# Kernel optimization log

Measured on AMD Instinct MI355X. Metric: run time of the kernel, lower is better.

The kernel has to match this reference:

```python
import jax, jax.numpy as jnp
import numpy as np

TOKENS = 4096
IN_FEATURES = 4096
OUT_FEATURES = 4096
NNZ = 512  # nonzeros per output row, multiple of 4 so vectorize-pad is a no-op


def setup_inputs() -> dict:
    key = jax.random.key(0)
    k1, k2, k3, k4 = jax.random.split(key, 4)
    x = jax.random.normal(k1, (TOKENS, IN_FEATURES), dtype=jnp.float32)
    w = jax.random.normal(k2, (OUT_FEATURES, NNZ), dtype=jnp.float32)
    # sorted per-row column indices, mimicking nonzero() order of a pruned row
    mask = jnp.sort(
        jax.random.randint(k3, (OUT_FEATURES, NNZ), 0, IN_FEATURES, dtype=jnp.int32),
        axis=-1,
    )
    b = jax.random.normal(k4, (OUT_FEATURES,), dtype=jnp.float32)
    return {"input": x, "condensed_weight": w, "input_mask": mask, "bias": b}


def reference(input, condensed_weight, input_mask, bias):
    # y[t, o] = sum_k input[t, input_mask[o, k]] * condensed_weight[o, k] + bias[o]
    # Scatter condensed rows back to a dense [O, In] weight, then GEMM.
    # .add handles duplicate / padded (index 0, weight 0) entries exactly like
    # the gather-multiply-reduce formulation.
    O, K = condensed_weight.shape
    In = input.shape[-1]
    rows = jnp.arange(O, dtype=input_mask.dtype)[:, None]  # [O, 1]
    W = jnp.zeros((O, In), dtype=condensed_weight.dtype).at[rows, input_mask].add(condensed_weight)
    return input @ W.T + bias
```

## Files before the change

### kernel.cpp

```cpp
#include <hip/hip_runtime.h>
#include <hip/hip_bf16.h>
#include <stdint.h>

#define TOKENS 4096
#define IN_F   4096
#define OUT_F  4096
#define NNZ    512

using floatx4 = __attribute__((ext_vector_type(4))) float;
using bf16x8  = __attribute__((ext_vector_type(8))) __bf16;

__device__ __forceinline__ unsigned short f2bf(float f) {
    unsigned int u = __float_as_uint(f);
    u += 0x7FFFu + ((u >> 16) & 1u);
    return (unsigned short)(u >> 16);
}

__global__ __launch_bounds__(256) void prep_fused(
        const float* __restrict__ x,
        const float* __restrict__ w,
        const int*   __restrict__ mask,
        unsigned short* __restrict__ Xb,
        unsigned short* __restrict__ Wb) {
    __shared__ unsigned short row[IN_F];
    const int b = blockIdx.x;
    const int t = threadIdx.x;

    if (b < OUT_F) {
        uint4* rv = (uint4*)row;
        rv[t]       = make_uint4(0u, 0u, 0u, 0u);
        rv[t + 256] = make_uint4(0u, 0u, 0u, 0u);
        __syncthreads();

        const int base = b * NNZ;
#pragma unroll
        for (int e = 0; e < 2; ++e) {
            const int k = t + e * 256;
            const int idx = mask[base + k];
            if (k == 0 || mask[base + k - 1] != idx) {
                float s = w[base + k];
                int j = k + 1;
                while (j < NNZ && mask[base + j] == idx) { s += w[base + j]; ++j; }
                row[idx] = f2bf(s);
            }
        }
        __syncthreads();

        uint4* out = (uint4*)(Wb + (size_t)b * IN_F);
        out[t]       = rv[t];
        out[t + 256] = rv[t + 256];
    } else {
        const int i = (b - OUT_F) * 256 + t;
        const float4* xv = (const float4*)x;
        float4 a = xv[2 * i];
        float4 c = xv[2 * i + 1];
        uint4 o;
        o.x = (unsigned)f2bf(a.x) | ((unsigned)f2bf(a.y) << 16);
        o.y = (unsigned)f2bf(a.z) | ((unsigned)f2bf(a.w) << 16);
        o.z = (unsigned)f2bf(c.x) | ((unsigned)f2bf(c.y) << 16);
        o.w = (unsigned)f2bf(c.z) | ((unsigned)f2bf(c.w) << 16);
        ((uint4*)Xb)[i] = o;
    }
}

__global__ __launch_bounds__(256) void gemm_bt_bias(
        const unsigned short* __restrict__ A,
        const unsigned short* __restrict__ B,
        const float* __restrict__ bias,
        float* __restrict__ C) {
    __shared__ unsigned short As[128 * 64];
    __shared__ unsigned short Bs[128 * 64];

    const int tid  = threadIdx.x;
    const int wave = tid >> 6;
    const int lane = tid & 63;
    const int m0 = blockIdx.y * 128;
    const int n0 = blockIdx.x * 128;
    const int wm = (wave >> 1) * 64;
    const int wn = (wave & 1) * 64;

    floatx4 acc[4][4] = {};

    const int lrow = lane >> 3;
    const int kseg = (lane & 7) ^ lrow;
    const int lq   = lane >> 4;
    const int lm   = lane & 15;
    const int lm7  = lm & 7;

    for (int k0 = 0; k0 < IN_F; k0 += 64) {
#pragma unroll
        for (int i = 0; i < 4; ++i) {
            const int cb  = (i * 4 + wave);
            const int row = cb * 8 + lrow;
            const unsigned short* ga =
                A + (size_t)(m0 + row) * IN_F + k0 + kseg * 8;
            const unsigned short* gb =
                B + (size_t)(n0 + row) * IN_F + k0 + kseg * 8;
            __builtin_amdgcn_global_load_lds(
                (__attribute__((address_space(1))) void*)ga,
                (__attribute__((address_space(3))) void*)(As + cb * 512),
                16, 0, 0);
            __builtin_amdgcn_global_load_lds(
                (__attribute__((address_space(1))) void*)gb,
                (__attribute__((address_space(3))) void*)(Bs + cb * 512),
                16, 0, 0);
        }
        __syncthreads();

#pragma unroll
        for (int ks = 0; ks < 2; ++ks) {
            bf16x8 af[4], bfr[4];
#pragma unroll
            for (int mi = 0; mi < 4; ++mi) {
                const int chunk = (ks * 4 + lq) ^ lm7;
                af[mi] = *(const bf16x8*)(As + (wm + mi * 16 + lm) * 64 + chunk * 8);
            }
#pragma unroll
            for (int ni = 0; ni < 4; ++ni) {
                const int chunk = (ks * 4 + lq) ^ lm7;
                bfr[ni] = *(const bf16x8*)(Bs + (wn + ni * 16 + lm) * 64 + chunk * 8);
            }
#pragma unroll
            for (int mi = 0; mi < 4; ++mi)
#pragma unroll
                for (int ni = 0; ni < 4; ++ni)
                    acc[mi][ni] = __builtin_amdgcn_mfma_f32_16x16x32_bf16(
                        af[mi], bfr[ni], acc[mi][ni], 0, 0, 0);
        }
        __syncthreads();
    }

#pragma unroll
    for (int ni = 0; ni < 4; ++ni) {
        const int n = n0 + wn + ni * 16 + lm;
        const float bv = bias[n];
#pragma unroll
        for (int mi = 0; mi < 4; ++mi) {
            const int mbase = m0 + wm + mi * 16 + lq * 4;
#pragma unroll
            for (int r = 0; r < 4; ++r) {
                C[(size_t)(mbase + r) * OUT_F + n] = acc[mi][ni][r] + bv;
            }
        }
    }
}

extern "C" void kernel_launch(void* const* d_in, const int* in_sizes, int n_in,
                              void* d_out, int out_size, void* d_ws, size_t ws_size,
                              hipStream_t stream) {
    const float* x    = (const float*)d_in[0];
    const float* w    = (const float*)d_in[1];
    const int*   mask = (const int*)d_in[2];
    const float* bias = (const float*)d_in[3];
    float* out = (float*)d_out;

    unsigned short* Xb = (unsigned short*)d_ws;
    unsigned short* Wb = Xb + (size_t)TOKENS * IN_F;

    prep_fused<<<OUT_F + 8192, 256, 0, stream>>>(x, w, mask, Xb, Wb);
    dim3 grid(32, 32);
    gemm_bt_bias<<<grid, 256, 0, stream>>>(Xb, Wb, bias, out);
}
```

Baseline: 281.2 us.

## Rewrite GEMM as 256x256 tile, 8-wave, double-buffered pipelined MFMA kernel

Measured after the change: 253.8 us. 1.11x faster.

```diff
diff --git a/kernel.cpp b/kernel.cpp
--- a/kernel.cpp
+++ b/kernel.cpp
@@ -63,83 +63,178 @@
     }
 }
 
-__global__ __launch_bounds__(256) void gemm_bt_bias(
+
+#define GLL16(src, dst) \
+    __builtin_amdgcn_global_load_lds((__attribute__((address_space(1))) void*)(src), \
+                                     (__attribute__((address_space(3))) void*)(dst), 16, 0, 0)
+
+__global__ __launch_bounds__(512, 2) void gemm_bt_bias(
         const unsigned short* __restrict__ A,
         const unsigned short* __restrict__ B,
         const float* __restrict__ bias,
         float* __restrict__ C) {
-    __shared__ unsigned short As[128 * 64];
-    __shared__ unsigned short Bs[128 * 64];
+    __shared__ unsigned short As[2][16384];
+    __shared__ unsigned short Bs[2][16384];
 
     const int tid  = threadIdx.x;
     const int wave = tid >> 6;
     const int lane = tid & 63;
-    const int m0 = blockIdx.y * 128;
-    const int n0 = blockIdx.x * 128;
-    const int wm = (wave >> 1) * 64;
-    const int wn = (wave & 1) * 64;
-
-    floatx4 acc[4][4] = {};
-
-    const int lrow = lane >> 3;
-    const int kseg = (lane & 7) ^ lrow;
     const int lq   = lane >> 4;
     const int lm   = lane & 15;
     const int lm7  = lm & 7;
-
-    for (int k0 = 0; k0 < IN_F; k0 += 64) {
-#pragma unroll
-        for (int i = 0; i < 4; ++i) {
-            const int cb  = (i * 4 + wave);
-            const int row = cb * 8 + lrow;
-            const unsigned short* ga =
-                A + (size_t)(m0 + row) * IN_F + k0 + kseg * 8;
-            const unsigned short* gb =
-                B + (size_t)(n0 + row) * IN_F + k0 + kseg * 8;
-            __builtin_amdgcn_global_load_lds(
-                (__attribute__((address_space(1))) void*)ga,
-                (__attribute__((address_space(3))) void*)(As + cb * 512),
-                16, 0, 0);
-            __builtin_amdgcn_global_load_lds(
-                (__attribute__((address_space(1))) void*)gb,
-                (__attribute__((address_space(3))) void*)(Bs + cb * 512),
-                16, 0, 0);
-        }
-        __syncthreads();
-
-#pragma unroll
-        for (int ks = 0; ks < 2; ++ks) {
-            bf16x8 af[4], bfr[4];
-#pragma unroll
-            for (int mi = 0; mi < 4; ++mi) {
-                const int chunk = (ks * 4 + lq) ^ lm7;
-                af[mi] = *(const bf16x8*)(As + (wm + mi * 16 + lm) * 64 + chunk * 8);
-            }
-#pragma unroll
-            for (int ni = 0; ni < 4; ++ni) {
-                const int chunk = (ks * 4 + lq) ^ lm7;
-                bfr[ni] = *(const bf16x8*)(Bs + (wn + ni * 16 + lm) * 64 + chunk * 8);
-            }
-#pragma unroll
-            for (int mi = 0; mi < 4; ++mi)
-#pragma unroll
-                for (int ni = 0; ni < 4; ++ni)
-                    acc[mi][ni] = __builtin_amdgcn_mfma_f32_16x16x32_bf16(
-                        af[mi], bfr[ni], acc[mi][ni], 0, 0, 0);
-        }
-        __syncthreads();
+    const int wm2  = wave >> 2;
+    const int wn4  = wave & 3;
+
+    const int bid = blockIdx.x;
+    const int swz = (bid & 7) * 32 + (bid >> 3);
+    const int m0  = (swz >> 4) << 8;
+    const int n0  = (swz & 15) << 8;
+
+    const int r   = tid >> 3;
+    const int cse = ((tid & 7) ^ (r & 7)) * 8;
+    const int oAX0 = (m0 + r)       * IN_F + cse;
+    const int oAX1 = (m0 + 128 + r) * IN_F + cse;
+    const int oAY0 = (m0 +  64 + r) * IN_F + cse;
+    const int oAY1 = (m0 + 192 + r) * IN_F + cse;
+    const int bc_  = (r >> 5) * 64 + (r & 31);
+    const int oBU0 = (n0 + bc_)        * IN_F + cse;
+    const int oBU1 = (n0 + 128 + bc_)  * IN_F + cse;
+    const int oBV0 = (n0 +  32 + bc_)  * IN_F + cse;
+    const int oBV1 = (n0 + 160 + bc_)  * IN_F + cse;
+    const int wofs = wave * 512;
+
+#define STAGE_AX(bb, kk) { GLL16(A + oAX0 + (kk), &As[bb][        wofs]); \
+                           GLL16(A + oAX1 + (kk), &As[bb][ 4096 + wofs]); }
+#define STAGE_AY(bb, kk) { GLL16(A + oAY0 + (kk), &As[bb][ 8192 + wofs]); \
+                           GLL16(A + oAY1 + (kk), &As[bb][12288 + wofs]); }
+#define STAGE_BU(bb, kk) { GLL16(B + oBU0 + (kk), &Bs[bb][        wofs]); \
+                           GLL16(B + oBU1 + (kk), &Bs[bb][ 4096 + wofs]); }
+#define STAGE_BV(bb, kk) { GLL16(B + oBV0 + (kk), &Bs[bb][ 8192 + wofs]); \
+                           GLL16(B + oBV1 + (kk), &Bs[bb][12288 + wofs]); }
+
+    const int ck0 = (lq ^ lm7) * 8;
+    const int ck1 = ck0 ^ 32;
+    const int aX  = (wm2 * 64 + lm) * 64;
+    const int aY  = aX + 8192;
+    const int bU  = (wn4 * 32 + lm) * 64;
+    const int bV  = bU + 8192;
+
+    floatx4 acc[8][4] = {};
+    bf16x8 af[4][2], bu[2][2], bv[2][2];
+
+    STAGE_AX(0, 0); STAGE_BU(0, 0); STAGE_BV(0, 0); STAGE_AY(0, 0);
+    STAGE_AX(1, 64); STAGE_BU(1, 64); STAGE_BV(1, 64);
+    asm volatile("s_waitcnt vmcnt(6)" ::: "memory");
+    __builtin_amdgcn_s_barrier();
+
+#define TILE_STEP(T, BB)                                                          \
+    {                                                                             \
+        const unsigned short* sA = As[BB];                                        \
+        const unsigned short* sB = Bs[BB];                                        \
+        const int kk1 = ((T) + 1 < 64 ? (T) + 1 : 63) * 64;                       \
+        const int kk2 = ((T) + 2 < 64 ? (T) + 2 : 63) * 64;                       \
+                                                      \
+        _Pragma("unroll")                                                         \
+        for (int mi = 0; mi < 4; ++mi) {                                          \
+            af[mi][0] = *(const bf16x8*)(sA + aX + mi * 1024 + ck0);              \
+            af[mi][1] = *(const bf16x8*)(sA + aX + mi * 1024 + ck1);              \
+        }                                                                         \
+        _Pragma("unroll")                                                         \
+        for (int ni = 0; ni < 2; ++ni) {                                          \
+            bu[ni][0] = *(const bf16x8*)(sB + bU + ni * 1024 + ck0);              \
+            bu[ni][1] = *(const bf16x8*)(sB + bU + ni * 1024 + ck1);              \
+        }                                                                         \
+        STAGE_AY((BB) ^ 1, kk1);                                                  \
+        asm volatile("s_waitcnt lgkmcnt(8)" ::: "memory");                        \
+        __builtin_amdgcn_s_barrier();                                             \
+        asm volatile("s_waitcnt lgkmcnt(0)" ::: "memory");                        \
+        __builtin_amdgcn_s_setprio(1);                                            \
+        _Pragma("unroll")                                                         \
+        for (int mi = 0; mi < 4; ++mi)                                            \
+            _Pragma("unroll")                                                     \
+            for (int ni = 0; ni < 2; ++ni) {                                      \
+                acc[mi][ni] = __builtin_amdgcn_mfma_f32_16x16x32_bf16(            \
+                    af[mi][0], bu[ni][0], acc[mi][ni], 0, 0, 0);                  \
+                acc[mi][ni] = __builtin_amdgcn_mfma_f32_16x16x32_bf16(            \
+                    af[mi][1], bu[ni][1], acc[mi][ni], 0, 0, 0);                  \
+            }                                                                     \
+        __builtin_amdgcn_s_setprio(0);                                            \
+        __builtin_amdgcn_s_barrier();                                             \
+                                                      \
+        _Pragma("unroll")                                                         \
+        for (int ni = 0; ni < 2; ++ni) {                                          \
+            bv[ni][0] = *(const bf16x8*)(sB + bV + ni * 1024 + ck0);              \
+            bv[ni][1] = *(const bf16x8*)(sB + bV + ni * 1024 + ck1);              \
+        }                                                                         \
+        STAGE_AX((BB), kk2);                                                      \
+        __builtin_amdgcn_s_barrier();                                             \
+        asm volatile("s_waitcnt lgkmcnt(0)" ::: "memory");                        \
+        __builtin_amdgcn_s_setprio(1);                                            \
+        _Pragma("unroll")                                                         \
+        for (int mi = 0; mi < 4; ++mi)                                            \
+            _Pragma("unroll")                                                     \
+            for (int ni = 0; ni < 2; ++ni) {                                      \
+                acc[mi][2 + ni] = __builtin_amdgcn_mfma_f32_16x16x32_bf16(        \
+                    af[mi][0], bv[ni][0], acc[mi][2 + ni], 0, 0, 0);              \
+                acc[mi][2 + ni] = __builtin_amdgcn_mfma_f32_16x16x32_bf16(        \
+                    af[mi][1], bv[ni][1], acc[mi][2 + ni], 0, 0, 0);              \
+            }                                                                     \
+        __builtin_amdgcn_s_setprio(0);                                            \
+        __builtin_amdgcn_s_barrier();                                             \
+                                                      \
+        _Pragma("unroll")                                                         \
+        for (int mi = 0; mi < 4; ++mi) {                                          \
+            af[mi][0] = *(const bf16x8*)(sA + aY + mi * 1024 + ck0);              \
+            af[mi][1] = *(const bf16x8*)(sA + aY + mi * 1024 + ck1);              \
+        }                                                                         \
+        STAGE_BU((BB), kk2);                                                      \
+        __builtin_amdgcn_s_barrier();                                             \
+        asm volatile("s_waitcnt lgkmcnt(0)" ::: "memory");                        \
+        __builtin_amdgcn_s_setprio(1);                                            \
+        _Pragma("unroll")                                                         \
+        for (int mi = 0; mi < 4; ++mi)                                            \
+            _Pragma("unroll")                                                     \
+            for (int ni = 0; ni < 2; ++ni) {                                      \
+                acc[4 + mi][2 + ni] = __builtin_amdgcn_mfma_f32_16x16x32_bf16(    \
+                    af[mi][0], bv[ni][0], acc[4 + mi][2 + ni], 0, 0, 0);          \
+                acc[4 + mi][2 + ni] = __builtin_amdgcn_mfma_f32_16x16x32_bf16(    \
+                    af[mi][1], bv[ni][1], acc[4 + mi][2 + ni], 0, 0, 0);          \
+            }                                                                     \
+        __builtin_amdgcn_s_setprio(0);                                            \
+        __builtin_amdgcn_s_barrier();                                             \
+                                \
+        STAGE_BV((BB), kk2);                                                      \
+        __builtin_amdgcn_s_barrier();                                             \
+        __builtin_amdgcn_s_setprio(1);                                            \
+        _Pragma("unroll")                                                         \
+        for (int mi = 0; mi < 4; ++mi)                                            \
+            _Pragma("unroll")                                                     \
+            for (int ni = 0; ni < 2; ++ni) {                                      \
+                acc[4 + mi][ni] = __builtin_amdgcn_mfma_f32_16x16x32_bf16(        \
+                    af[mi][0], bu[ni][0], acc[4 + mi][ni], 0, 0, 0);              \
+                acc[4 + mi][ni] = __builtin_amdgcn_mfma_f32_16x16x32_bf16(        \
+                    af[mi][1], bu[ni][1], acc[4 + mi][ni], 0, 0, 0);              \
+            }                                                                     \
+        __builtin_amdgcn_s_setprio(0);                                            \
+        asm volatile("s_waitcnt vmcnt(6)" ::: "memory");                          \
+        __builtin_amdgcn_s_barrier();                                             \
+    }
+
+    for (int tt = 0; tt < 32; ++tt) {
+        TILE_STEP(2 * tt,     0);
+        TILE_STEP(2 * tt + 1, 1);
     }
 
 #pragma unroll
     for (int ni = 0; ni < 4; ++ni) {
-        const int n = n0 + wn + ni * 16 + lm;
-        const float bv = bias[n];
-#pragma unroll
-        for (int mi = 0; mi < 4; ++mi) {
-            const int mbase = m0 + wm + mi * 16 + lq * 4;
-#pragma unroll
-            for (int r = 0; r < 4; ++r) {
-                C[(size_t)(mbase + r) * OUT_F + n] = acc[mi][ni][r] + bv;
+        const int n = n0 + wn4 * 64 + ni * 16 + lm;
+        const float bb = bias[n];
+#pragma unroll
+        for (int mi = 0; mi < 8; ++mi) {
+            const int mb = m0 + wm2 * 128 + mi * 16 + lq * 4;
+#pragma unroll
+            for (int rr = 0; rr < 4; ++rr) {
+                C[(size_t)(mb + rr) * OUT_F + n] = acc[mi][ni][rr] + bb;
             }
         }
     }
@@ -158,6 +253,5 @@
     unsigned short* Wb = Xb + (size_t)TOKENS * IN_F;
 
     prep_fused<<<OUT_F + 8192, 256, 0, stream>>>(x, w, mask, Xb, Wb);
-    dim3 grid(32, 32);
-    gemm_bt_bias<<<grid, 256, 0, stream>>>(Xb, Wb, bias, out);
-}
+    gemm_bt_bias<<<dim3(256), dim3(512), 0, stream>>>(Xb, Wb, bias, out);
+}
```
